# Performance work log

Measured on AMD Instinct MI355X. Metric: run time of the kernel, lower is better.

## Reference

```python
import jax, jax.numpy as jnp
import numpy as np

HEADS = 2
BN_EPS = 1e-5


def _upsample2x_bilinear_ac(x):
    # torch nn.Upsample(scale_factor=2, mode='bilinear', align_corners=True)
    B, C, H, W = x.shape

    def grid(n):
        c = jnp.arange(2 * n) * ((n - 1) / (2 * n - 1))  # align_corners mapping
        i0 = jnp.clip(jnp.floor(c).astype(jnp.int32), 0, n - 2)
        w = (c - i0).astype(x.dtype)
        return i0, w

    i0, wh = grid(H)
    j0, ww = grid(W)
    x = x[:, :, i0, :] * (1 - wh)[None, None, :, None] + x[:, :, i0 + 1, :] * wh[None, None, :, None]
    x = x[:, :, :, j0] * (1 - ww) + x[:, :, :, j0 + 1] * ww
    return x


def _self_attn(x, wq, wkv, wo, wob):
    # x: (b, t, d); lucidrains axial_attention SelfAttention
    b, t, d = x.shape
    e = d // HEADS
    q = x @ wq
    k, v = jnp.split(x @ wkv, 2, axis=-1)
    mh = lambda z: z.reshape(b, t, HEADS, e).transpose(0, 2, 1, 3)  # (b,h,t,e)
    q, k, v = mh(q), mh(k), mh(v)
    dots = jnp.einsum('bhie,bhje->bhij', q, k) * (e ** -0.5)
    attn = jax.nn.softmax(dots, axis=-1)
    o = jnp.einsum('bhij,bhje->bhie', attn, v)
    o = o.transpose(0, 2, 1, 3).reshape(b, t, d)
    return o @ wo + wob


def setup_inputs() -> dict:
    key = jax.random.key(0)
    ks = jax.random.split(key, 16)
    C, E = 256, 128
    cat = 2 * C + E
    s = 0.02
    inp = {
        'x': jax.random.normal(ks[0], (4, C, 64, 64), jnp.float32),
        'res': jax.random.normal(ks[1], (4, E, 128, 128), jnp.float32),
        'wq_h': jax.random.normal(ks[2], (C, C), jnp.float32) * s,
        'wkv_h': jax.random.normal(ks[3], (C, 2 * C), jnp.float32) * s,
        'wo_h': jax.random.normal(ks[4], (C, C), jnp.float32) * s,
        'wob_h': jnp.zeros((C,), jnp.float32),
        'wq_w': jax.random.normal(ks[5], (C, C), jnp.float32) * s,
        'wkv_w': jax.random.normal(ks[6], (C, 2 * C), jnp.float32) * s,
        'wo_w': jax.random.normal(ks[7], (C, C), jnp.float32) * s,
        'wob_w': jnp.zeros((C,), jnp.float32),
        'conv_w': jax.random.normal(ks[8], (cat, E), jnp.float32) * s,
        'gamma': jnp.ones((E,), jnp.float32),
        'beta': jnp.zeros((E,), jnp.float32),
    }
    return inp


def reference(x, res, wq_h, wkv_h, wo_h, wob_h, wq_w, wkv_w, wo_w, wob_w, conv_w, gamma, beta):
    xu = _upsample2x_bilinear_ac(x)  # (B,C,2H,2W)
    B, C, H, W = xu.shape
    # axial attention along H (rows): batch over B*W
    ah = xu.transpose(0, 3, 2, 1).reshape(B * W, H, C)
    ah = _self_attn(ah, wq_h, wkv_h, wo_h, wob_h).reshape(B, W, H, C).transpose(0, 3, 2, 1)
    # axial attention along W (cols): batch over B*H
    aw = xu.transpose(0, 2, 3, 1).reshape(B * H, W, C)
    aw = _self_attn(aw, wq_w, wkv_w, wo_w, wob_w).reshape(B, H, W, C).transpose(0, 3, 1, 2)
    x_attn = jax.nn.relu(ah + aw)  # sum_axial_out=True, then ReLU
    cat = jnp.concatenate([x_attn, xu, res], axis=1)  # (B, 2C+E, H, W)
    y = jnp.einsum('bchw,ce->behw', cat, conv_w)  # conv1x1, no bias
    y = jax.nn.relu(y)
    # BatchNorm2d, training-mode batch stats (biased variance)
    mu = y.mean(axis=(0, 2, 3), keepdims=True)
    var = y.var(axis=(0, 2, 3), keepdims=True)
    y = (y - mu) / jnp.sqrt(var + BN_EPS)
    return y * gamma[None, :, None, None] + beta[None, :, None, None]
```

## Files before the change

kernel.cpp:

```cpp
#include <hip/hip_runtime.h>
#include <hip/hip_bf16.h>
#include <cstdio>


typedef short bf16x8 __attribute__((ext_vector_type(8)));
typedef short bf16x4 __attribute__((ext_vector_type(4)));
typedef float f32x4 __attribute__((ext_vector_type(4)));

#define MFMA16(a, b, c) __builtin_amdgcn_mfma_f32_16x16x32_bf16((a), (b), (c), 0, 0, 0)

__device__ __forceinline__ short f2bf(float v) {
  __hip_bfloat16 h = __float2bfloat16(v);
  union { __hip_bfloat16 h; short s; } u; u.h = h; return u.s;
}
__device__ __forceinline__ float bf2f(short s) {
  return __uint_as_float(((unsigned int)(unsigned short)s) << 16);
}
__device__ __forceinline__ int swz(int row, int col) {
  return col ^ ((row & 7) << 3);
}

struct WtAll {
  const float* src[7];
  short* dst[7];
  int K[7], N[7], tile0[7];
};

__global__ __launch_bounds__(256) void k_wt_all(WtAll P) {
  const int bid = blockIdx.x;
  int i = 0;
#pragma unroll
  for (int j = 1; j < 7; j++) if (bid >= P.tile0[j]) i = j;
  const float* src = P.src[i];
  short* dst = P.dst[i];
  const int K = P.K[i], N = P.N[i];
  const int local = bid - P.tile0[i];
  const int ktiles = K >> 5;
  const int nt = local / ktiles, kt = local - nt * ktiles;
  const int k0 = kt * 32, n0 = nt * 32;
  __shared__ float tile[32][33];
  const int tx = threadIdx.x & 31, ty = threadIdx.x >> 5;
#pragma unroll
  for (int r = 0; r < 4; r++)
    tile[ty + r * 8][tx] = src[(size_t)(k0 + ty + r * 8) * N + n0 + tx];
  __syncthreads();
#pragma unroll
  for (int r = 0; r < 4; r++)
    dst[(size_t)(n0 + ty + r * 8) * K + k0 + tx] = f2bf(tile[tx][ty + r * 8]);
}

__global__ __launch_bounds__(256) void k_upsample(const float* __restrict__ x,
                                                  short* __restrict__ xu) {
  __shared__ float ldsV[64][65];
  const int bh = blockIdx.x, z = blockIdx.y;
  const int b = bh >> 7, h = bh & 127;
  const float chf = h * (63.0f / 127.0f);
  int i0 = (int)chf; if (i0 > 62) i0 = 62;
  const float wh = chf - (float)i0;
  const int t = threadIdx.x;
  const int cbase = z * 64;
  const float* xb = x + ((size_t)(b * 256 + cbase) * 64 + i0) * 64;
#pragma unroll
  for (int p = 0; p < 16; p++) {
    const int li = p * 256 + t;
    const int c = li >> 6, w = li & 63;
    const float* px = xb + (size_t)c * 4096 + w;
    const float v0 = px[0], v1 = px[64];
    ldsV[c][w] = v0 * (1.f - wh) + v1 * wh;
  }
  __syncthreads();
  const int cg = t & 7, wi = t >> 3;
  short* xout = xu + (size_t)(bh * 128) * 256 + cbase + cg * 8;
#pragma unroll
  for (int p = 0; p < 4; p++) {
    const int w = p * 32 + wi;
    const float cwf = w * (63.0f / 127.0f);
    int j0 = (int)cwf; if (j0 > 62) j0 = 62;
    const float ww = cwf - (float)j0;
    bf16x8 o;
#pragma unroll
    for (int u = 0; u < 8; u++) {
      const float v0 = ldsV[cg * 8 + u][j0], v1 = ldsV[cg * 8 + u][j0 + 1];
      o[u] = f2bf(v0 * (1.f - ww) + v1 * ww);
    }
    *(bf16x8*)(xout + (size_t)w * 256) = o;
  }
}

__global__ __launch_bounds__(512, 2) void k_fused(const short* __restrict__ xu,
                                                  const short* __restrict__ wqkvT0,
                                                  const short* __restrict__ woT0,
                                                  const float* __restrict__ wob0,
                                                  const float* __restrict__ wob1,
                                                  short* __restrict__ accb0,
                                                  short* __restrict__ accb1) {
  __shared__ __align__(16) short Xs[128][256];
  __shared__ __align__(16) short Qb[128][128];
  __shared__ __align__(16) short Kb[128][128];
  __shared__ __align__(16) short Vtb[128][128];

  const int dir = blockIdx.y;
  const short* wqkvT = wqkvT0 + (size_t)dir * 196608;
  const short* woT   = woT0 + (size_t)dir * 65536;
  const float* wob   = dir ? wob1 : wob0;
  short* accb        = dir ? accb1 : accb0;

  const int s = blockIdx.x;
  const int b = s >> 7, pos = s & 127;
  const int tok0 = b * 16384 + (dir ? pos * 128 : pos);
  const int tstep = dir ? 1 : 128;
  const int tid = threadIdx.x;
  const int lane = tid & 63, wid = tid >> 6;
  const int lr = lane & 15, kb = lane >> 4;
  const int ct = wid * 16;
  const float scale = 0.08838834764831845f;

#pragma unroll
  for (int p = 0; p < 8; p++) {
    const int u = p * 512 + tid;
    const int row = u >> 5, ck = (u & 31) * 8;
    bf16x8 v = *(const bf16x8*)(xu + (size_t)(tok0 + row * tstep) * 256 + ck);
    *(bf16x8*)&Xs[row][swz(row, ck)] = v;
  }

  f32x4 accp[2][8];
#pragma unroll
  for (int i = 0; i < 2; i++)
#pragma unroll
    for (int j = 0; j < 8; j++) accp[i][j] = (f32x4){0.f, 0.f, 0.f, 0.f};

  for (int h = 0; h < 2; h++) {
    const short* wqb = wqkvT + (size_t)(h * 128 + ct + lr) * 256 + kb * 8;
    const short* wkb = wqkvT + (size_t)(256 + h * 128 + ct + lr) * 256 + kb * 8;
    const short* wvb = wqkvT + (size_t)(512 + h * 128 + ct + lr) * 256 + kb * 8;
    bf16x8 wq[8], wk[8], wv[8];
#pragma unroll
    for (int ks = 0; ks < 8; ks++) {
      wq[ks] = *(const bf16x8*)(wqb + ks * 32);
      wk[ks] = *(const bf16x8*)(wkb + ks * 32);
      wv[ks] = *(const bf16x8*)(wvb + ks * 32);
    }

    __syncthreads();

#pragma unroll
    for (int nt = 0; nt < 8; nt++) {
      const int xrow = nt * 16 + lr;
      f32x4 dq = (f32x4){0.f, 0.f, 0.f, 0.f};
      f32x4 dk = (f32x4){0.f, 0.f, 0.f, 0.f};
      f32x4 dv = (f32x4){0.f, 0.f, 0.f, 0.f};
#pragma unroll
      for (int ks = 0; ks < 8; ks++) {
        bf16x8 xf = *(const bf16x8*)&Xs[xrow][swz(xrow, kb * 8 + ks * 32)];
        dq = MFMA16(wq[ks], xf, dq);
        dk = MFMA16(wk[ks], xf, dk);
        dv = MFMA16(xf, wv[ks], dv);
      }
      const int trow = nt * 16 + lr, cc = ct + kb * 4;
      bf16x4 pq = {f2bf(dq[0]), f2bf(dq[1]), f2bf(dq[2]), f2bf(dq[3])};
      bf16x4 pk = {f2bf(dk[0]), f2bf(dk[1]), f2bf(dk[2]), f2bf(dk[3])};
      *(bf16x4*)&Qb[trow][swz(trow, cc)] = pq;
      *(bf16x4*)&Kb[trow][swz(trow, cc)] = pk;
      const int vrow = ct + lr;
      bf16x4 pv = {f2bf(dv[0]), f2bf(dv[1]), f2bf(dv[2]), f2bf(dv[3])};
      *(bf16x4*)&Vtb[vrow][swz(vrow, nt * 16 + kb * 4)] = pv;
    }

    __syncthreads();

    f32x4 s8[8];
#pragma unroll
    for (int i = 0; i < 8; i++) s8[i] = (f32x4){0.f, 0.f, 0.f, 0.f};
    const int qrow = ct + lr;
#pragma unroll
    for (int ks = 0; ks < 4; ks++) {
      bf16x8 aq = *(const bf16x8*)&Qb[qrow][swz(qrow, kb * 8 + ks * 32)];
#pragma unroll
      for (int nj = 0; nj < 8; nj++) {
        const int krow = nj * 16 + lr;
        bf16x8 bk = *(const bf16x8*)&Kb[krow][swz(krow, kb * 8 + ks * 32)];
        s8[nj] = MFMA16(bk, aq, s8[nj]);
      }
    }
    {
      float m = s8[0][0];
#pragma unroll
      for (int nj = 0; nj < 8; nj++)
#pragma unroll
        for (int r = 0; r < 4; r++) m = fmaxf(m, s8[nj][r]);
      m = fmaxf(m, __shfl_xor(m, 16));
      m = fmaxf(m, __shfl_xor(m, 32));
      float sum = 0.f;
#pragma unroll
      for (int nj = 0; nj < 8; nj++)
#pragma unroll
        for (int r = 0; r < 4; r++) {
          s8[nj][r] = __expf((s8[nj][r] - m) * scale);
          sum += s8[nj][r];
        }
      sum += __shfl_xor(sum, 16);
      sum += __shfl_xor(sum, 32);
      const float inv = 1.f / sum;
#pragma unroll
      for (int nj = 0; nj < 8; nj++) {
        bf16x4 pp = {f2bf(s8[nj][0] * inv), f2bf(s8[nj][1] * inv),
                     f2bf(s8[nj][2] * inv), f2bf(s8[nj][3] * inv)};
        *(bf16x4*)&Qb[qrow][swz(qrow, nj * 16 + kb * 4)] = pp;
      }
    }

    f32x4 o8[8];
#pragma unroll
    for (int i = 0; i < 8; i++) o8[i] = (f32x4){0.f, 0.f, 0.f, 0.f};
#pragma unroll
    for (int ks = 0; ks < 4; ks++) {
      bf16x8 bp = *(const bf16x8*)&Qb[qrow][swz(qrow, kb * 8 + ks * 32)];
#pragma unroll
      for (int mi = 0; mi < 8; mi++) {
        const int vrow = mi * 16 + lr;
        bf16x8 av = *(const bf16x8*)&Vtb[vrow][swz(vrow, kb * 8 + ks * 32)];
        o8[mi] = MFMA16(av, bp, o8[mi]);
      }
    }

    __syncthreads();

#pragma unroll
    for (int mi = 0; mi < 8; mi++) {
      const int cc = mi * 16 + kb * 4;
      bf16x4 po = {f2bf(o8[mi][0]), f2bf(o8[mi][1]), f2bf(o8[mi][2]), f2bf(o8[mi][3])};
      *(bf16x4*)&Kb[qrow][swz(qrow, cc)] = po;
    }

    __syncthreads();

    {
      const short* w0 = woT + (size_t)(wid * 32 + lr) * 256 + h * 128 + kb * 8;
      const short* w1 = woT + (size_t)(wid * 32 + 16 + lr) * 256 + h * 128 + kb * 8;
      bf16x8 wa[4], wb2[4];
#pragma unroll
      for (int ks = 0; ks < 4; ks++) {
        wa[ks]  = *(const bf16x8*)(w0 + ks * 32);
        wb2[ks] = *(const bf16x8*)(w1 + ks * 32);
      }
#pragma unroll
      for (int nt = 0; nt < 8; nt++) {
        const int trow = nt * 16 + lr;
#pragma unroll
        for (int ks = 0; ks < 4; ks++) {
          bf16x8 bo = *(const bf16x8*)&Kb[trow][swz(trow, kb * 8 + ks * 32)];
          accp[0][nt] = MFMA16(wa[ks], bo, accp[0][nt]);
          accp[1][nt] = MFMA16(wb2[ks], bo, accp[1][nt]);
        }
      }
    }
  }

#pragma unroll
  for (int mi2 = 0; mi2 < 2; mi2++) {
    const int outc = wid * 32 + mi2 * 16 + kb * 4;
    const float b0 = wob[outc], b1 = wob[outc + 1];
    const float b2 = wob[outc + 2], b3 = wob[outc + 3];
#pragma unroll
    for (int nt = 0; nt < 8; nt++) {
      const int token = tok0 + (nt * 16 + lr) * tstep;
      bf16x4 pv = {f2bf(accp[mi2][nt][0] + b0), f2bf(accp[mi2][nt][1] + b1),
                   f2bf(accp[mi2][nt][2] + b2), f2bf(accp[mi2][nt][3] + b3)};
      *(bf16x4*)(accb + (size_t)token * 256 + outc) = pv;
    }
  }
}

__global__ __launch_bounds__(256) void k_gemm_conv(const short* __restrict__ accb0,
                                                   const short* __restrict__ accb1,
                                                   const short* __restrict__ xu,
                                                   const float* __restrict__ res,
                                                   const short* __restrict__ Bt,
                                                   float* __restrict__ ytmp,
                                                   float* __restrict__ partial) {
  __shared__ float redS[2][128], redS2[2][128];
  const int tid = threadIdx.x;
  const int lane = tid & 63, wid = tid >> 6;
  const int lr = lane & 15, kb = lane >> 4;
  const int wr = wid >> 1, wc = wid & 1;
  const int m0 = blockIdx.y * 128;
  f32x4 acc[4][4];
#pragma unroll
  for (int i = 0; i < 4; i++)
#pragma unroll
    for (int j = 0; j < 4; j++) acc[i][j] = (f32x4){0.f, 0.f, 0.f, 0.f};
  const short* arow0 = accb0 + (size_t)(m0 + wr * 64 + lr) * 256 + kb * 8;
  const short* arow1 = accb1 + (size_t)(m0 + wr * 64 + lr) * 256 + kb * 8;
  const short* arow2 = xu + (size_t)(m0 + wr * 64 + lr) * 256 + kb * 8;
  const short* brow = Bt + (size_t)(wc * 64 + lr) * 640 + kb * 8;
#pragma unroll
  for (int ks = 0; ks < 8; ks++) {
    bf16x8 a[4], b[4];
#pragma unroll
    for (int mi = 0; mi < 4; mi++) {
      bf16x8 t0 = *(const bf16x8*)(arow0 + (size_t)mi * 16 * 256 + ks * 32);
      bf16x8 t1 = *(const bf16x8*)(arow1 + (size_t)mi * 16 * 256 + ks * 32);
      bf16x8 tv;
#pragma unroll
      for (int u = 0; u < 8; u++) {
        float sv = bf2f(t0[u]) + bf2f(t1[u]);
        tv[u] = f2bf(fmaxf(sv, 0.f));
      }
      a[mi] = tv;
    }
#pragma unroll
    for (int nj = 0; nj < 4; nj++)
      b[nj] = *(const bf16x8*)(brow + (size_t)nj * 16 * 640 + ks * 32);
#pragma unroll
    for (int mi = 0; mi < 4; mi++)
#pragma unroll
      for (int nj = 0; nj < 4; nj++)
        acc[mi][nj] = MFMA16(a[mi], b[nj], acc[mi][nj]);
  }
#pragma unroll
  for (int ks = 8; ks < 16; ks++) {
    bf16x8 a[4], b[4];
#pragma unroll
    for (int mi = 0; mi < 4; mi++)
      a[mi] = *(const bf16x8*)(arow2 + (size_t)mi * 16 * 256 + (ks - 8) * 32);
#pragma unroll
    for (int nj = 0; nj < 4; nj++)
      b[nj] = *(const bf16x8*)(brow + (size_t)nj * 16 * 640 + ks * 32);
#pragma unroll
    for (int mi = 0; mi < 4; mi++)
#pragma unroll
      for (int nj = 0; nj < 4; nj++)
        acc[mi][nj] = MFMA16(a[mi], b[nj], acc[mi][nj]);
  }
  const int bC = (m0 >> 14) * 128;
  const int hh = (m0 >> 7) & 127;
#pragma unroll
  for (int ks = 16; ks < 20; ks++) {
    const int e0 = (ks - 16) * 32 + kb * 8;
    bf16x8 a[4], b[4];
#pragma unroll
    for (int mi = 0; mi < 4; mi++) {
      const int wl = wr * 64 + mi * 16 + lr;
      const float* rp = res + ((size_t)(bC + e0) * 128 + hh) * 128 + wl;
      bf16x8 tv;
#pragma unroll
      for (int u = 0; u < 8; u++) tv[u] = f2bf(rp[(size_t)u * 16384]);
      a[mi] = tv;
    }
#pragma unroll
    for (int nj = 0; nj < 4; nj++)
      b[nj] = *(const bf16x8*)(brow + (size_t)nj * 16 * 640 + ks * 32);
#pragma unroll
    for (int mi = 0; mi < 4; mi++)
#pragma unroll
      for (int nj = 0; nj < 4; nj++)
        acc[mi][nj] = MFMA16(a[mi], b[nj], acc[mi][nj]);
  }
#pragma unroll
  for (int nj = 0; nj < 4; nj++) {
    float s = 0.f, s2 = 0.f;
    const int c = wc * 64 + nj * 16 + lr;
#pragma unroll
    for (int mi = 0; mi < 4; mi++) {
      const int rbase = m0 + wr * 64 + mi * 16 + kb * 4;
#pragma unroll
      for (int r = 0; r < 4; r++) {
        const float yv = fmaxf(acc[mi][nj][r], 0.f);
        ytmp[(size_t)(rbase + r) * 128 + c] = yv;
        s += yv; s2 += yv * yv;
      }
    }
    s += __shfl_xor(s, 16);  s += __shfl_xor(s, 32);
    s2 += __shfl_xor(s2, 16); s2 += __shfl_xor(s2, 32);
    if (kb == 0) { redS[wr][c] = s; redS2[wr][c] = s2; }
  }
  __syncthreads();
  if (tid < 128) {
    partial[((size_t)blockIdx.y * 128 + tid) * 2]     = redS[0][tid] + redS[1][tid];
    partial[((size_t)blockIdx.y * 128 + tid) * 2 + 1] = redS2[0][tid] + redS2[1][tid];
  }
}

__global__ __launch_bounds__(128) void k_bnstats2(const float* __restrict__ partial,
                                                  float* __restrict__ stats) {
  const int ch = threadIdx.x;
  float s = 0.f, s2 = 0.f;
  for (int i = 0; i < 512; i++) {
    s  += partial[(size_t)(i * 128 + ch) * 2];
    s2 += partial[(size_t)(i * 128 + ch) * 2 + 1];
  }
  const float mu = s * (1.f / 65536.f);
  const float var = s2 * (1.f / 65536.f) - mu * mu;
  stats[ch * 2] = mu;
  stats[ch * 2 + 1] = rsqrtf(var + 1e-5f);
}

__global__ __launch_bounds__(256) void k_bnout(const float* __restrict__ y,
                                               const float* __restrict__ stats,
                                               const float* __restrict__ gamma,
                                               const float* __restrict__ beta,
                                               float* __restrict__ out) {
  const int bh = blockIdx.x;
  const int b = bh >> 7, h = bh & 127;
  const int w = threadIdx.x & 127, half = threadIdx.x >> 7;
  const float* yp = y + (size_t)(bh * 128 + w) * 128 + half * 64;
  float* op = out + ((size_t)(b * 128) << 14) + h * 128 + w;
#pragma unroll
  for (int e4 = 0; e4 < 16; e4++) {
    f32x4 v = *(const f32x4*)(yp + e4 * 4);
#pragma unroll
    for (int u = 0; u < 4; u++) {
      const int e = half * 64 + e4 * 4 + u;
      const float mu = stats[e * 2], rstd = stats[e * 2 + 1];
      op[(size_t)e << 14] = (v[u] - mu) * rstd * gamma[e] + beta[e];
    }
  }
}

extern "C" void kernel_launch(void* const* d_in, const int* in_sizes, int n_in,
                              void* d_out, int out_size, void* d_ws, size_t ws_size,
                              hipStream_t stream) {
  const float* x      = (const float*)d_in[0];
  const float* res    = (const float*)d_in[1];
  const float* wq_h   = (const float*)d_in[2];
  const float* wkv_h  = (const float*)d_in[3];
  const float* wo_h   = (const float*)d_in[4];
  const float* wob_h  = (const float*)d_in[5];
  const float* wq_w   = (const float*)d_in[6];
  const float* wkv_w  = (const float*)d_in[7];
  const float* wo_w   = (const float*)d_in[8];
  const float* wob_w  = (const float*)d_in[9];
  const float* conv_w = (const float*)d_in[10];
  const float* gamma  = (const float*)d_in[11];
  const float* beta   = (const float*)d_in[12];

  char* ws = (char*)d_ws;
  short* wqkvT[2] = {(short*)(ws + 0), (short*)(ws + 393216)};
  short* woT[2]   = {(short*)(ws + 786432), (short*)(ws + 917504)};
  short* convT    = (short*)(ws + 1048576);
  short* xu       = (short*)(ws + 1245184);
  float* ytmp     = (float*)(ws + 34799616);
  float* partial  = (float*)(ws + 68354048);
  float* stats    = (float*)(ws + 68878336);
  short* accb1    = (short*)(ws + 68879360);
  short* accb0    = (short*)d_out;
  float* out      = (float*)d_out;

  if (ws_size < 102433792ull)
    fprintf(stderr, "kernel_launch: ws_size %zu too small\n", ws_size);

  WtAll P;
  P.src[0] = wq_h;  P.dst[0] = wqkvT[0];          P.K[0] = 256; P.N[0] = 256; P.tile0[0] = 0;
  P.src[1] = wkv_h; P.dst[1] = wqkvT[0] + 65536;  P.K[1] = 256; P.N[1] = 512; P.tile0[1] = 64;
  P.src[2] = wq_w;  P.dst[2] = wqkvT[1];          P.K[2] = 256; P.N[2] = 256; P.tile0[2] = 192;
  P.src[3] = wkv_w; P.dst[3] = wqkvT[1] + 65536;  P.K[3] = 256; P.N[3] = 512; P.tile0[3] = 256;
  P.src[4] = wo_h;  P.dst[4] = woT[0];            P.K[4] = 256; P.N[4] = 256; P.tile0[4] = 384;
  P.src[5] = wo_w;  P.dst[5] = woT[1];            P.K[5] = 256; P.N[5] = 256; P.tile0[5] = 448;
  P.src[6] = conv_w;P.dst[6] = convT;             P.K[6] = 640; P.N[6] = 128; P.tile0[6] = 512;
  k_wt_all<<<592, 256, 0, stream>>>(P);

  k_upsample<<<dim3(512, 4), 256, 0, stream>>>(x, xu);

  k_fused<<<dim3(512, 2), 512, 0, stream>>>(xu, wqkvT[0], woT[0],
                                            wob_h, wob_w, accb0, accb1);

  k_gemm_conv<<<dim3(1, 512), 256, 0, stream>>>(accb0, accb1, xu, res, convT,
                                                ytmp, partial);
  k_bnstats2<<<1, 128, 0, stream>>>(partial, stats);
  k_bnout<<<512, 256, 0, stream>>>(ytmp, stats, gamma, beta, out);
}
```

Measured before the change: 247.9 us.

## Store conv output as bf16, parallelize BN stats, reuse Q buffer for attention output

After: 229.1 us. -7.6%, faster.

```diff
diff --git a/kernel.cpp b/kernel.cpp
--- a/kernel.cpp
+++ b/kernel.cpp
@@ -223,13 +223,11 @@
       }
     }
 
-    __syncthreads();
-
 #pragma unroll
     for (int mi = 0; mi < 8; mi++) {
       const int cc = mi * 16 + kb * 4;
       bf16x4 po = {f2bf(o8[mi][0]), f2bf(o8[mi][1]), f2bf(o8[mi][2]), f2bf(o8[mi][3])};
-      *(bf16x4*)&Kb[qrow][swz(qrow, cc)] = po;
+      *(bf16x4*)&Qb[qrow][swz(qrow, cc)] = po;
     }
 
     __syncthreads();
@@ -248,7 +246,7 @@
         const int trow = nt * 16 + lr;
 #pragma unroll
         for (int ks = 0; ks < 4; ks++) {
-          bf16x8 bo = *(const bf16x8*)&Kb[trow][swz(trow, kb * 8 + ks * 32)];
+          bf16x8 bo = *(const bf16x8*)&Qb[trow][swz(trow, kb * 8 + ks * 32)];
           accp[0][nt] = MFMA16(wa[ks], bo, accp[0][nt]);
           accp[1][nt] = MFMA16(wb2[ks], bo, accp[1][nt]);
         }
@@ -276,7 +274,7 @@
                                                    const short* __restrict__ xu,
                                                    const float* __restrict__ res,
                                                    const short* __restrict__ Bt,
-                                                   float* __restrict__ ytmp,
+                                                   short* __restrict__ ytmp,
                                                    float* __restrict__ partial) {
   __shared__ float redS[2][128], redS2[2][128];
   const int tid = threadIdx.x;
@@ -366,7 +364,7 @@
 #pragma unroll
       for (int r = 0; r < 4; r++) {
         const float yv = fmaxf(acc[mi][nj][r], 0.f);
-        ytmp[(size_t)(rbase + r) * 128 + c] = yv;
+        ytmp[(size_t)(rbase + r) * 128 + c] = f2bf(yv);
         s += yv; s2 += yv * yv;
       }
     }
@@ -381,21 +379,29 @@
   }
 }
 
-__global__ __launch_bounds__(128) void k_bnstats2(const float* __restrict__ partial,
-                                                  float* __restrict__ stats) {
-  const int ch = threadIdx.x;
+__global__ __launch_bounds__(64) void k_bnstats2(const float* __restrict__ partial,
+                                                 float* __restrict__ stats) {
+  const int ch = blockIdx.x;
+  const int t = threadIdx.x;
   float s = 0.f, s2 = 0.f;
-  for (int i = 0; i < 512; i++) {
+  for (int i = t; i < 512; i += 64) {
     s  += partial[(size_t)(i * 128 + ch) * 2];
     s2 += partial[(size_t)(i * 128 + ch) * 2 + 1];
   }
-  const float mu = s * (1.f / 65536.f);
-  const float var = s2 * (1.f / 65536.f) - mu * mu;
-  stats[ch * 2] = mu;
-  stats[ch * 2 + 1] = rsqrtf(var + 1e-5f);
-}
-
-__global__ __launch_bounds__(256) void k_bnout(const float* __restrict__ y,
+#pragma unroll
+  for (int d = 1; d < 64; d <<= 1) {
+    s  += __shfl_xor(s, d);
+    s2 += __shfl_xor(s2, d);
+  }
+  if (t == 0) {
+    const float mu = s * (1.f / 65536.f);
+    const float var = s2 * (1.f / 65536.f) - mu * mu;
+    stats[ch * 2] = mu;
+    stats[ch * 2 + 1] = rsqrtf(var + 1e-5f);
+  }
+}
+
+__global__ __launch_bounds__(256) void k_bnout(const short* __restrict__ y,
                                                const float* __restrict__ stats,
                                                const float* __restrict__ gamma,
                                                const float* __restrict__ beta,
@@ -403,16 +409,16 @@
   const int bh = blockIdx.x;
   const int b = bh >> 7, h = bh & 127;
   const int w = threadIdx.x & 127, half = threadIdx.x >> 7;
-  const float* yp = y + (size_t)(bh * 128 + w) * 128 + half * 64;
+  const short* yp = y + (size_t)(bh * 128 + w) * 128 + half * 64;
   float* op = out + ((size_t)(b * 128) << 14) + h * 128 + w;
 #pragma unroll
-  for (int e4 = 0; e4 < 16; e4++) {
-    f32x4 v = *(const f32x4*)(yp + e4 * 4);
-#pragma unroll
-    for (int u = 0; u < 4; u++) {
-      const int e = half * 64 + e4 * 4 + u;
+  for (int e8 = 0; e8 < 8; e8++) {
+    bf16x8 v = *(const bf16x8*)(yp + e8 * 8);
+#pragma unroll
+    for (int u = 0; u < 8; u++) {
+      const int e = half * 64 + e8 * 8 + u;
       const float mu = stats[e * 2], rstd = stats[e * 2 + 1];
-      op[(size_t)e << 14] = (v[u] - mu) * rstd * gamma[e] + beta[e];
+      op[(size_t)e << 14] = (bf2f(v[u]) - mu) * rstd * gamma[e] + beta[e];
     }
   }
 }
@@ -439,14 +445,14 @@
   short* woT[2]   = {(short*)(ws + 786432), (short*)(ws + 917504)};
   short* convT    = (short*)(ws + 1048576);
   short* xu       = (short*)(ws + 1245184);
-  float* ytmp     = (float*)(ws + 34799616);
-  float* partial  = (float*)(ws + 68354048);
-  float* stats    = (float*)(ws + 68878336);
-  short* accb1    = (short*)(ws + 68879360);
+  short* ytmp     = (short*)(ws + 34799616);
+  float* partial  = (float*)(ws + 51576832);
+  float* stats    = (float*)(ws + 52101120);
+  short* accb1    = (short*)(ws + 52102144);
   short* accb0    = (short*)d_out;
   float* out      = (float*)d_out;
 
-  if (ws_size < 102433792ull)
+  if (ws_size < 85656576ull)
     fprintf(stderr, "kernel_launch: ws_size %zu too small\n", ws_size);
 
   WtAll P;
@@ -466,6 +472,6 @@
 
   k_gemm_conv<<<dim3(1, 512), 256, 0, stream>>>(accb0, accb1, xu, res, convT,
                                                 ytmp, partial);
-  k_bnstats2<<<1, 128, 0, stream>>>(partial, stats);
+  k_bnstats2<<<128, 64, 0, stream>>>(partial, stats);
   k_bnout<<<512, 256, 0, stream>>>(ytmp, stats, gamma, beta, out);
 }
```
